# Optimization experiments

Hardware: AMD Instinct MI355X
Metric: run time of the kernel (lower is better)

The kernel has to match this reference:

```python
import jax, jax.numpy as jnp
import numpy as np
from jax import lax

STRIDES = [8, 16, 32, 64, 128]
NUM_CLASSES = 80
PRE_NMS_THRESH = 0.05
PRE_NMS_TOP_N = 1000
NMS_THRESH = 0.6
MAX_DET = 100
IMG_SIZE = 800.0
BBOX_W = (10.0, 10.0, 5.0, 5.0)
SCALE_CLAMP = float(np.log(1000.0 / 16.0))  # Box2BoxTransform clamp


def conv3x3(x, w, b):
    y = lax.conv_general_dilated(x, w, (1, 1), 'SAME',
                                 dimension_numbers=('NCHW', 'OIHW', 'NCHW'))
    return y + b[None, :, None, None]


def conv1x1(x, w, b):
    return jnp.einsum('nchw,kc->nkhw', x, w) + b[None, :, None, None]


def make_anchors(H, W, stride):
    # one square anchor per location, size = 8 * stride (ATSS), offset 0.5
    size = 8.0 * stride
    xs = (jnp.arange(W, dtype=jnp.float32) + 0.5) * stride
    ys = (jnp.arange(H, dtype=jnp.float32) + 0.5) * stride
    cy, cx = jnp.meshgrid(ys, xs, indexing='ij')
    half = size / 2.0
    return jnp.stack([cx - half, cy - half, cx + half, cy + half], -1).reshape(-1, 4)


def decode(deltas, anchors):
    # Box2BoxTransform.apply_deltas with weights (10,10,5,5)
    wx, wy, ww, wh = BBOX_W
    aw = anchors[..., 2] - anchors[..., 0]
    ah = anchors[..., 3] - anchors[..., 1]
    acx = anchors[..., 0] + 0.5 * aw
    acy = anchors[..., 1] + 0.5 * ah
    dx = deltas[..., 0] / wx
    dy = deltas[..., 1] / wy
    dw = jnp.minimum(deltas[..., 2] / ww, SCALE_CLAMP)
    dh = jnp.minimum(deltas[..., 3] / wh, SCALE_CLAMP)
    pcx = dx * aw + acx
    pcy = dy * ah + acy
    pw = jnp.exp(dw) * aw
    ph = jnp.exp(dh) * ah
    boxes = jnp.stack([pcx - 0.5 * pw, pcy - 0.5 * ph,
                       pcx + 0.5 * pw, pcy + 0.5 * ph], -1)
    return jnp.clip(boxes, 0.0, IMG_SIZE)


def iou_one_vs_all(box, boxes):
    x1 = jnp.maximum(box[0], boxes[:, 0])
    y1 = jnp.maximum(box[1], boxes[:, 1])
    x2 = jnp.minimum(box[2], boxes[:, 2])
    y2 = jnp.minimum(box[3], boxes[:, 3])
    inter = jnp.clip(x2 - x1, 0.0) * jnp.clip(y2 - y1, 0.0)
    a1 = (box[2] - box[0]) * (box[3] - box[1])
    a2 = (boxes[:, 2] - boxes[:, 0]) * (boxes[:, 3] - boxes[:, 1])
    return inter / (a1 + a2 - inter + 1e-9)


def nms_single(boxes, scores, classes):
    # class-aware greedy NMS via per-class coordinate offset (ml_nms trick)
    off = classes.astype(boxes.dtype)[:, None] * (2.0 * IMG_SIZE)
    ob = boxes + off

    def step(s, _):
        i = jnp.argmax(s)
        best = s[i]
        iou = iou_one_vs_all(ob[i], ob)
        s = jnp.where(iou > NMS_THRESH, -1.0, s)
        s = s.at[i].set(-1.0)
        return s, (i, best)

    _, (idx, kept) = lax.scan(step, scores, None, length=MAX_DET)
    valid = kept > 0
    out_boxes = jnp.where(valid[:, None], boxes[idx], 0.0)
    out_scores = jnp.where(valid, kept, 0.0)
    out_classes = jnp.where(valid, classes[idx], -1)
    return out_boxes, out_scores, out_classes


def atss_forward(feats, cls_tw, cls_tb, bbox_tw, bbox_tb,
                 wcls, bcls, wbox, bbox_b, wctr, bctr, scales):
    all_boxes, all_scores, all_classes = [], [], []
    for l, x in enumerate(feats):
        c = x
        b = x
        for i in range(cls_tw.shape[0]):  # 4 tower convs
            c = jax.nn.relu(conv3x3(c, cls_tw[i], cls_tb[i]))
            b = jax.nn.relu(conv3x3(b, bbox_tw[i], bbox_tb[i]))
        logits = conv1x1(c, wcls, bcls)               # [N,C,H,W]
        deltas = scales[l] * conv1x1(b, wbox, bbox_b)  # [N,4,H,W]
        ctr = conv1x1(b, wctr, bctr)                   # [N,1,H,W]
        N, C, H, W = logits.shape
        logits = logits.transpose(0, 2, 3, 1).reshape(N, H * W, C)
        deltas = deltas.transpose(0, 2, 3, 1).reshape(N, H * W, 4)
        ctr = ctr.transpose(0, 2, 3, 1).reshape(N, H * W)
        anchors = make_anchors(H, W, STRIDES[l])       # [HW,4]
        # ATSS inference scoring: sigmoid(cls) * sigmoid(centerness)
        s = jax.nn.sigmoid(logits) * jax.nn.sigmoid(ctr)[..., None]
        s = jnp.where(s > PRE_NMS_THRESH, s, 0.0)
        flat = s.reshape(N, -1)                        # [N, HW*C]
        k = min(PRE_NMS_TOP_N, flat.shape[1])
        vals, idx = lax.top_k(flat, k)
        aidx = idx // C
        cidx = idx % C
        d = jnp.take_along_axis(deltas, aidx[:, :, None], axis=1)  # [N,k,4]
        boxes = decode(d, anchors[aidx])
        # final score = sqrt(cls*ctr); safe sqrt to avoid inf grad at 0
        sc = jnp.sqrt(jnp.where(vals > 0, vals, 1.0)) * (vals > 0)
        all_boxes.append(boxes)
        all_scores.append(sc)
        all_classes.append(cidx)
    boxes = jnp.concatenate(all_boxes, 1)
    scores = jnp.concatenate(all_scores, 1)
    classes = jnp.concatenate(all_classes, 1)
    return jax.vmap(nms_single)(boxes, scores, classes)


def setup_inputs() -> dict:
    key = jax.random.key(0)
    ks = jax.random.split(key, 12)
    feats_hw = [(100, 100), (50, 50), (25, 25), (13, 13), (7, 7)]
    N, CIN, CH = 4, 256, 256
    inp = {}
    for i, (h, w) in enumerate(feats_hw):
        inp['p%d' % (i + 3)] = jax.random.normal(ks[i], (N, CIN, h, w), jnp.float32)
    inp['cls_tw'] = jax.random.normal(ks[5], (4, CH, CIN, 3, 3), jnp.float32) * 0.02
    inp['cls_tb'] = jnp.zeros((4, CH), jnp.float32)
    inp['bbox_tw'] = jax.random.normal(ks[6], (4, CH, CIN, 3, 3), jnp.float32) * 0.02
    inp['bbox_tb'] = jnp.zeros((4, CH), jnp.float32)
    inp['wcls'] = jax.random.normal(ks[7], (NUM_CLASSES, CH), jnp.float32) * 0.05
    inp['bcls'] = jnp.zeros((NUM_CLASSES,), jnp.float32)
    inp['wbox'] = jax.random.normal(ks[8], (4, CH), jnp.float32) * 0.05
    inp['bbox_b'] = jnp.zeros((4,), jnp.float32)
    inp['wctr'] = jax.random.normal(ks[9], (1, CH), jnp.float32) * 0.05
    inp['bctr'] = jnp.zeros((1,), jnp.float32)
    inp['scales'] = jnp.ones((5,), jnp.float32)
    return inp


def reference(p3, p4, p5, p6, p7, cls_tw, cls_tb, bbox_tw, bbox_tb,
              wcls, bcls, wbox, bbox_b, wctr, bctr, scales):
    feats = [p3, p4, p5, p6, p7]
    boxes, scores, classes = atss_forward(feats, cls_tw, cls_tb, bbox_tw, bbox_tb,
                                          wcls, bcls, wbox, bbox_b, wctr, bctr, scales)
    return boxes, scores, classes
```

## Files before the change

kernel.cpp:

```cpp
#include <hip/hip_runtime.h>
#include <math.h>

typedef short s8v __attribute__((ext_vector_type(8)));
typedef short s4v __attribute__((ext_vector_type(4)));
typedef float f4v __attribute__((ext_vector_type(4)));
typedef _Float16 h8v __attribute__((ext_vector_type(8)));

__device__ __forceinline__ float sigf(float x) { return 1.f / (1.f + expf(-x)); }
__device__ __forceinline__ float f16f(short v) {
  return (float)__builtin_bit_cast(_Float16, v);
}

#define SCALE_CLAMP 4.135166556742356f
#define IMG_SIZE 800.f
#define PLANE 14482432ull
#define W_SCALE 1024.f
#define A_SCALE 64.f
#define ACC_RESCALE 1.52587890625e-5f

__device__ __forceinline__ void split2(float x, short& h, short& l) {
  _Float16 hf = (_Float16)x;
  _Float16 lf = (_Float16)(x - (float)hf);
  h = __builtin_bit_cast(short, hf);
  l = __builtin_bit_cast(short, lf);
}

struct Geo {
  int tp[6];
  int TXa[5];
  int Ha[5], Wa[5], PWa[5], PHWa[5];
  int phwOff[5];
  int hwOff[5];
  int pb[6];
  int bb[6];
};

__global__ __launch_bounds__(256) void wtrans_k(const float* __restrict__ cls_tw,
                                                const float* __restrict__ bbox_tw,
                                                short* __restrict__ wt)
{
  const int total = 589824;
  for (int u = blockIdx.x * 256 + threadIdx.x; u < total; u += gridDim.x * 256) {
    int layer = u / 73728;
    int r = u - layer * 73728;
    int tap = r / 8192;  r -= tap * 8192;
    int cc  = r / 1024;  r -= cc * 1024;
    int qq  = r / 256;   int ko = r - qq * 256;
    int cibase = cc * 32 + qq * 8;
    const float* src = (layer < 4) ? (cls_tw + (size_t)layer * 589824)
                                   : (bbox_tw + (size_t)(layer - 4) * 589824);
    s8v hv, lv;
#pragma unroll
    for (int e = 0; e < 8; ++e) {
      float x = src[(size_t)ko * 2304 + (size_t)(cibase + e) * 9 + tap] * W_SCALE;
      short h, l; split2(x, h, l);
      hv[e] = h; lv[e] = l;
    }
    size_t dbase = (size_t)layer * 1179648 + (((size_t)tap * 8 + cc) * 4 + qq) * 2048 + (size_t)ko * 8;
    *(s8v*)(wt + dbase) = hv;
    *(s8v*)(wt + dbase + 589824) = lv;
  }
}

__global__ __launch_bounds__(256) void prep_all_k(const float* __restrict__ p3, const float* __restrict__ p4,
                                                  const float* __restrict__ p5, const float* __restrict__ p6,
                                                  const float* __restrict__ p7,
                                                  short* __restrict__ out, Geo g)
{
  __shared__ float tl[64][260];
  int bx = blockIdx.x, t = threadIdx.x, n = blockIdx.y;
  int l = 0; while (l < 4 && bx >= g.pb[l + 1]) ++l;
  const float* in = (l == 0) ? p3 : (l == 1) ? p4 : (l == 2) ? p5 : (l == 3) ? p6 : p7;
  int H = g.Ha[l], W = g.Wa[l], PW = g.PWa[l], PHW = g.PHWa[l], HW = H * W;
  int P0 = (bx - g.pb[l]) * 64;
  const float* inN = in + (size_t)n * HW * 256;
  int sub = t >> 6, pl = t & 63;
  int pos = P0 + pl;
  for (int i = 0; i < 64; ++i) {
    int ci = i * 4 + sub;
    tl[pl][ci] = (pos < HW) ? inN[(size_t)ci * HW + pos] : 0.f;
  }
  __syncthreads();
  int pl2 = t >> 2, cq = (t & 3) * 64;
  int pos2 = P0 + pl2;
  if (pos2 < HW) {
    int y = pos2 / W, x = pos2 - y * W;
    size_t oo = ((size_t)g.phwOff[l] * 4 + (size_t)n * PHW + (size_t)(y + 1) * PW + (x + 1)) * 256 + cq;
#pragma unroll
    for (int grp = 0; grp < 8; ++grp) {
      s8v hv, lv;
#pragma unroll
      for (int e = 0; e < 8; ++e) {
        short h, lo; split2(tl[pl2][cq + grp * 8 + e] * A_SCALE, h, lo);
        hv[e] = h; lv[e] = lo;
      }
      *(s8v*)(out + oo + grp * 8) = hv;
      *(s8v*)(out + PLANE + oo + grp * 8) = lv;
    }
  }
}

#define QS    112
#define QVALID 108
#define PSTR  3584
#define BSTR  7168
__global__ __launch_bounds__(256, 4) void conv_all_k(const short* __restrict__ in0,
                                                     const short* __restrict__ in1,
                                                     const short* __restrict__ wt0,
                                                     const short* __restrict__ wt1,
                                                     const float* __restrict__ bias0,
                                                     const float* __restrict__ bias1,
                                                     short* __restrict__ out0,
                                                     short* __restrict__ out1, Geo g)
{
  __shared__ short act_s[2 * BSTR];

  const int t = threadIdx.x;
  const int lane = t & 63, wave = t >> 6;
  const int wcol = wave & 1, wko = wave >> 1;
  const int tower = blockIdx.z >> 2;
  const int n = blockIdx.z & 3;
  const short* in   = tower ? in1 : in0;
  const short* wtL  = tower ? wt1 : wt0;
  const float* bias = tower ? bias1 : bias0;
  short* out        = tower ? out1 : out0;
  const int ko0 = blockIdx.y * 128;
  int bx = blockIdx.x;
  int l = 0; while (l < 4 && bx >= g.tp[l + 1]) ++l;
  const int H = g.Ha[l], W = g.Wa[l], PW = g.PWa[l], PHW = g.PHWa[l];
  const int lt = bx - g.tp[l];
  const int TX = g.TXa[l];
  const int ty = lt / TX, tx = lt - ty * TX;
  const int R0 = ty * 4, C0 = tx * 16;
  const size_t bi = ((size_t)g.phwOff[l] * 4 + (size_t)n * PHW) * 256;
  const short* inN = in + bi;
  short* outN = out + bi;

  const int r = lane & 15, q = lane >> 4;
  const int cb = wcol * 8;
  const short* wlane = wtL + (size_t)q * 2048 + (size_t)(ko0 + wko * 64 + r) * 8;

  int soff[2];
#pragma unroll
  for (int k = 0; k < 2; ++k) {
    int j = t + k * 256; if (j > 447) j = 447;
    int qq = j / QS, ppos = j - qq * QS;
    int lpos = ppos - 2 * qq; if (lpos < 0) lpos += QS;
    if (lpos >= QVALID) lpos = QVALID - 1;
    int row = lpos / 18, col = lpos - row * 18;
    int prow = R0 + row; if (prow > H + 1) prow = H + 1;
    int pcol = C0 + col; if (pcol > W + 1) pcol = W + 1;
    soff[k] = (prow * PW + pcol) * 256 + qq * 8;
  }

  f4v acc[2][4];
#pragma unroll
  for (int mi = 0; mi < 2; ++mi)
#pragma unroll
    for (int ni = 0; ni < 4; ++ni) { f4v z = {0.f, 0.f, 0.f, 0.f}; acc[mi][ni] = z; }

  auto stage = [&](int cc, int buf) {
#pragma unroll
    for (int k = 0; k < 2; ++k) {
      int j = t + k * 256;
      if (j < 448) {
#pragma unroll
        for (int p = 0; p < 2; ++p) {
          const short* src = inN + (size_t)p * PLANE + (size_t)(soff[k] + cc * 32);
          short* dst = &act_s[(size_t)buf * BSTR + (size_t)p * PSTR + (size_t)j * 8];
#if __has_builtin(__builtin_amdgcn_global_load_lds)
          __builtin_amdgcn_global_load_lds((const __attribute__((address_space(1))) void*)src,
                                           (__attribute__((address_space(3))) void*)dst, 16, 0, 0);
#else
          *(s8v*)dst = *(const s8v*)src;
#endif
        }
      }
    }
  };

  auto loadW = [&](s8v (&w)[2][2], int cc2, int tap2, int half) {
    const short* base = wlane + (size_t)(tap2 * 8 + cc2) * 8192 + half * 256;
#pragma unroll
    for (int p = 0; p < 2; ++p)
#pragma unroll
      for (int k = 0; k < 2; ++k)
        w[p][k] = *(const s8v*)(base + (size_t)p * 589824 + k * 128);
  };

  auto loadA = [&](s8v (&af)[2][2], int dy, int dx, int buf) {
    const int sbase = buf * BSTR;
#pragma unroll
    for (int mi = 0; mi < 2; ++mi) {
      int lp = (2 * mi + (r >> 3) + dy) * 18 + (cb + (r & 7) + dx) + 2 * q;
      if (lp >= QS) lp -= QS;
      int sl = q * QS + lp;
      af[0][mi] = *(const s8v*)&act_s[sbase + sl * 8];
      af[1][mi] = *(const s8v*)&act_s[sbase + PSTR + sl * 8];
    }
  };

  auto runHalf = [&](const s8v (&w)[2][2], const s8v (&af)[2][2], int half) {
    const int PA[3] = {0, 0, 1};
    const int PB[3] = {0, 1, 0};
    __builtin_amdgcn_s_setprio(1);
#pragma unroll
    for (int pp = 0; pp < 3; ++pp)
#pragma unroll
      for (int mi = 0; mi < 2; ++mi)
#pragma unroll
        for (int k = 0; k < 2; ++k)
          acc[mi][half * 2 + k] = __builtin_amdgcn_mfma_f32_16x16x32_f16(
              __builtin_bit_cast(h8v, af[PA[pp]][mi]),
              __builtin_bit_cast(h8v, w[PB[pp]][k]),
              acc[mi][half * 2 + k], 0, 0, 0);
    __builtin_amdgcn_s_setprio(0);
  };

  s8v wH0[2][2], wH1[2][2], afr[2][2];
  stage(0, 0);
  loadW(wH0, 0, 0, 0);
  __syncthreads();

  int cur = 0;
  for (int cc = 0; cc < 8; ++cc) {
    if (cc < 7) stage(cc + 1, cur ^ 1);
#pragma unroll
    for (int tap = 0; tap < 9; ++tap) {
      const int dy = tap / 3, dx = tap - dy * 3;
      loadW(wH1, cc, tap, 1);
      loadA(afr, dy, dx, cur);
      runHalf(wH0, afr, 0);
      int ntap = tap + 1, ncc = cc;
      if (ntap == 9) { ntap = 0; ++ncc; }
      if (ncc < 8) loadW(wH0, ncc, ntap, 0);
      runHalf(wH1, afr, 1);
    }
    __syncthreads();
    cur ^= 1;
  }

#pragma unroll
  for (int mi = 0; mi < 2; ++mi) {
#pragma unroll
    for (int ni = 0; ni < 4; ++ni) {
      int ko = ko0 + wko * 64 + ni * 16 + r;
      float bv = bias[ko];
#pragma unroll
      for (int reg = 0; reg < 4; ++reg) {
        int rm = q * 4 + reg;
        int orow = R0 + 2 * mi + (rm >> 3);
        int ocol = C0 + cb + (rm & 7);
        if (orow < H && ocol < W) {
          float real = acc[mi][ni][reg] * ACC_RESCALE + bv;
          float vv = fmaxf(real, 0.f) * A_SCALE;
          short h, lo; split2(vv, h, lo);
          size_t oo = ((size_t)(orow + 1) * PW + (ocol + 1)) * 256 + ko;
          outN[oo] = h; outN[PLANE + oo] = lo;
        }
      }
    }
  }
}

__global__ __launch_bounds__(256) void cls_head_k(const short* __restrict__ act,
                                                  const float* __restrict__ wcls,
                                                  const float* __restrict__ bcls,
                                                  float* __restrict__ score, Geo g)
{
  __shared__ int   p2s[64];
  __shared__ float as_[64][69];
  __shared__ float ws_[64][84];
  const int t = threadIdx.x;
  const int n = blockIdx.y;
  int bx = blockIdx.x;
  int l = 0; while (l < 4 && bx >= g.pb[l + 1]) ++l;
  const int H = g.Ha[l], W = g.Wa[l], PW = g.PWa[l], PHW = g.PHWa[l], HW = H * W;
  const int P0 = (bx - g.pb[l]) * 64;
  if (t < 64) {
    int p = P0 + t; if (p >= HW) p = HW - 1;
    int y = p / W, x = p - y * W;
    p2s[t] = (y + 1) * PW + x + 1;
  }
  __syncthreads();
  float accv[4][5];
#pragma unroll
  for (int i = 0; i < 4; ++i)
#pragma unroll
    for (int j = 0; j < 5; ++j) accv[i][j] = 0.f;

  const short* actN = act + ((size_t)g.phwOff[l] * 4 + (size_t)n * PHW) * 256;
  const int pg = t >> 4, cg = t & 15;
  const float inv = 1.f / A_SCALE;

  for (int c0 = 0; c0 < 256; c0 += 64) {
    for (int i = t; i < 1024; i += 256) {
      int pos = i >> 4, c4 = i & 15;
      size_t o = (size_t)p2s[pos] * 256 + c0 + c4 * 4;
      s4v hv = *(const s4v*)(actN + o);
      s4v lv = *(const s4v*)(actN + PLANE + o);
      float* dst = &as_[pos][c4 * 4];
#pragma unroll
      for (int e = 0; e < 4; ++e) dst[e] = (f16f(hv[e]) + f16f(lv[e])) * inv;
    }
    for (int i = t; i < 1280; i += 256) {
      int c = i >> 4, c4 = i & 15;
      float4 v = *(const float4*)(wcls + (size_t)c * 256 + c0 + c4 * 4);
      ws_[c4 * 4 + 0][c] = v.x; ws_[c4 * 4 + 1][c] = v.y;
      ws_[c4 * 4 + 2][c] = v.z; ws_[c4 * 4 + 3][c] = v.w;
    }
    __syncthreads();
#pragma unroll 8
    for (int ci = 0; ci < 64; ++ci) {
#pragma unroll
      for (int i = 0; i < 4; ++i) {
        float a = as_[pg * 4 + i][ci];
#pragma unroll
        for (int j = 0; j < 5; ++j)
          accv[i][j] = fmaf(a, ws_[ci][cg * 5 + j], accv[i][j]);
      }
    }
    __syncthreads();
  }
  float* sB = score + ((size_t)g.hwOff[l] * 4 + (size_t)n * HW) * 80;
#pragma unroll
  for (int i = 0; i < 4; ++i) {
    int p = P0 + pg * 4 + i;
    if (p >= HW) continue;
#pragma unroll
    for (int j = 0; j < 5; ++j) {
      int c = cg * 5 + j;
      sB[(size_t)p * 80 + c] = sigf(accv[i][j] + bcls[c]);
    }
  }
}

__global__ __launch_bounds__(256) void box_head_k(const short* __restrict__ act,
                                                  const float* __restrict__ wbox,
                                                  const float* __restrict__ bb,
                                                  const float* __restrict__ wctr,
                                                  const float* __restrict__ bc,
                                                  const float* __restrict__ scales,
                                                  float* __restrict__ score,
                                                  float* __restrict__ deltas, Geo g)
{
  int n = blockIdx.y;
  int bx = blockIdx.x;
  int l = 0; while (l < 4 && bx >= g.bb[l + 1]) ++l;
  const int H = g.Ha[l], W = g.Wa[l], PW = g.PWa[l], PHW = g.PHWa[l], HW = H * W;
  int p = (bx - g.bb[l]) * 256 + threadIdx.x;
  if (p >= HW) return;
  int y = p / W, x = p - y * W;
  const short* a = act + ((size_t)g.phwOff[l] * 4 + (size_t)n * PHW + (size_t)(y + 1) * PW + x + 1) * 256;
  const float inv = 1.f / A_SCALE;
  float d0 = 0, d1 = 0, d2 = 0, d3 = 0, ct = 0;
  for (int gI = 0; gI < 32; ++gI) {
    s8v hv = *(const s8v*)(a + gI * 8);
    s8v lv = *(const s8v*)(a + PLANE + gI * 8);
#pragma unroll
    for (int e = 0; e < 8; ++e) {
      float av = (f16f(hv[e]) + f16f(lv[e])) * inv;
      int c = gI * 8 + e;
      d0 = fmaf(av, wbox[c], d0);
      d1 = fmaf(av, wbox[256 + c], d1);
      d2 = fmaf(av, wbox[512 + c], d2);
      d3 = fmaf(av, wbox[768 + c], d3);
      ct = fmaf(av, wctr[c], ct);
    }
  }
  float sl = scales[l];
  float* dd = deltas + ((size_t)g.hwOff[l] * 4 + (size_t)n * HW + p) * 4;
  dd[0] = sl * (d0 + bb[0]); dd[1] = sl * (d1 + bb[1]);
  dd[2] = sl * (d2 + bb[2]); dd[3] = sl * (d3 + bb[3]);
  float sct = sigf(ct + bc[0]);
  float* sp = score + ((size_t)g.hwOff[l] * 4 + (size_t)n * HW + p) * 80;
#pragma unroll
  for (int i = 0; i < 20; ++i) {
    float4 v = ((float4*)sp)[i];
    v.x *= sct; v.y *= sct; v.z *= sct; v.w *= sct;
    v.x = (v.x > 0.05f) ? v.x : 0.f;
    v.y = (v.y > 0.05f) ? v.y : 0.f;
    v.z = (v.z > 0.05f) ? v.z : 0.f;
    v.w = (v.w > 0.05f) ? v.w : 0.f;
    ((float4*)sp)[i] = v;
  }
}

__global__ __launch_bounds__(256) void hist_k(const float* __restrict__ score,
                                              const unsigned* __restrict__ thr,
                                              unsigned* __restrict__ hist, int phase, Geo g)
{
  const int grp = blockIdx.y;
  const int l = grp >> 2, n = grp & 3;
  const int HW = g.Ha[l] * g.Wa[l];
  const int M = HW * 80;
  const float* s = score + ((size_t)g.hwOff[l] * 4 + (size_t)n * HW) * 80;
  unsigned* h = hist + grp * 2048;
  const unsigned* tr = thr + grp * 8;
  __shared__ unsigned lh[2048];
  for (int i = threadIdx.x; i < 2048; i += 256) lh[i] = 0u;
  __syncthreads();
  unsigned B1 = 0, pref = 0;
  if (phase == 1) B1 = tr[0];
  if (phase == 2) pref = (tr[0] << 11) | tr[1];
  for (int idx = blockIdx.x * 256 + threadIdx.x; idx < M; idx += gridDim.x * 256) {
    float v = s[idx];
    if (v > 0.f) {
      unsigned b = __float_as_uint(v);
      if (phase == 0) atomicAdd(&lh[b >> 20], 1u);
      else if (phase == 1) { if ((b >> 20) == B1) atomicAdd(&lh[(b >> 9) & 0x7FFu], 1u); }
      else { if ((b >> 9) == pref) atomicAdd(&lh[b & 0x1FFu], 1u); }
    }
  }
  __syncthreads();
  for (int i = threadIdx.x; i < 2048; i += 256) { unsigned v = lh[i]; if (v) atomicAdd(&h[i], v); }
}

__global__ __launch_bounds__(256) void scan_k(unsigned* __restrict__ hist,
                                              unsigned* __restrict__ thr, int phase)
{
  const int grp = blockIdx.x, t = threadIdx.x;
  unsigned* h  = hist + grp * 2048;
  unsigned* tr = thr + grp * 8;
  const int nb = (phase == 2) ? 512 : 2048;
  const int PB = nb / 256;
  unsigned target = 1000u;
  bool dead = false;
  if (phase >= 1) {
    target = 1000u - tr[2];
    if (tr[0] == 0xFFFFFFFFu) dead = true;
    if (phase == 2 && tr[1] == 0xFFFFFFFFu) dead = true;
  }
  __shared__ unsigned ps[256];
  __shared__ unsigned s_tot;
  const int hi = nb - t * PB;
  unsigned lsum = 0;
  for (int k = 0; k < PB; ++k) lsum += h[hi - 1 - k];
  ps[t] = lsum;
  __syncthreads();
  if (t == 0) {
    unsigned cum = 0;
    for (int i = 0; i < 256; ++i) { unsigned tmp = ps[i]; ps[i] = cum; cum += tmp; }
    s_tot = cum;
  }
  __syncthreads();
  unsigned exc = ps[t], tot = s_tot;
  if (!dead && tot >= target) {
    if (exc < target && exc + lsum >= target) {
      unsigned cum = exc; int bf = 0; unsigned above = 0;
      for (int k = 0; k < PB; ++k) {
        int bidx = hi - 1 - k;
        unsigned c = h[bidx];
        if (cum < target && cum + c >= target) { bf = bidx; above = cum; }
        cum += c;
      }
      if (phase == 0)      { tr[0] = (unsigned)bf; tr[2] = above; }
      else if (phase == 1) { tr[1] = (unsigned)bf; tr[2] = tr[2] + above; }
      else {
        unsigned T = (tr[0] << 20) | (tr[1] << 9) | (unsigned)bf;
        tr[3] = T; tr[4] = target - above;
      }
    }
  } else if (t == 0) {
    if (phase == 0)      { tr[0] = 0xFFFFFFFFu; tr[2] = 0u; }
    else if (phase == 1) { tr[1] = 0xFFFFFFFFu; }
    else                 { tr[3] = 0u; tr[4] = 0u; }
  }
  if (phase == 2 && t == 0) { tr[5] = 0u; tr[6] = 0u; }
}

__global__ __launch_bounds__(256) void select_k(const float* __restrict__ score,
                                                const float* __restrict__ deltas,
                                                unsigned* __restrict__ thr,
                                                float* __restrict__ cbox, float* __restrict__ csc,
                                                float* __restrict__ ccls, float* __restrict__ cgid,
                                                Geo g)
{
  const int grp = blockIdx.y;
  const int l = grp >> 2, n = grp & 3;
  const int W = g.Wa[l];
  const int HW = g.Ha[l] * W;
  const int M = HW * 80;
  const float stride_ = (float)(8 << l);
  const float* s = score + ((size_t)g.hwOff[l] * 4 + (size_t)n * HW) * 80;
  const float* dBase = deltas + ((size_t)g.hwOff[l] * 4 + (size_t)n * HW) * 4;
  unsigned* tr = thr + grp * 8;
  const unsigned T = tr[3], need = tr[4];
  for (int idx = blockIdx.x * 256 + threadIdx.x; idx < M; idx += gridDim.x * 256) {
    float v = s[idx];
    if (!(v > 0.f)) continue;
    unsigned b = __float_as_uint(v);
    int slot = -1;
    if (b > T) slot = (int)atomicAdd(&tr[5], 1u);
    else if (b == T) {
      unsigned e = atomicAdd(&tr[6], 1u);
      if (e < need) slot = (int)(1000u - need + e);
    }
    if (slot < 0) continue;
    int p = idx / 80, c = idx - p * 80;
    int y = p / W, x = p - y * W;
    const float* d = dBase + (size_t)p * 4;
    float sz  = 8.f * stride_;
    float acx = ((float)x + 0.5f) * stride_;
    float acy = ((float)y + 0.5f) * stride_;
    float dx = d[0] / 10.f, dy = d[1] / 10.f;
    float dw = fminf(d[2] / 5.f, SCALE_CLAMP);
    float dh = fminf(d[3] / 5.f, SCALE_CLAMP);
    float pcx = dx * sz + acx;
    float pcy = dy * sz + acy;
    float pw = expf(dw) * sz;
    float ph = expf(dh) * sz;
    float x1 = pcx - 0.5f * pw, y1_ = pcy - 0.5f * ph;
    float x2 = pcx + 0.5f * pw, y2_ = pcy + 0.5f * ph;
    x1  = fminf(fmaxf(x1, 0.f),  IMG_SIZE);
    y1_ = fminf(fmaxf(y1_, 0.f), IMG_SIZE);
    x2  = fminf(fmaxf(x2, 0.f),  IMG_SIZE);
    y2_ = fminf(fmaxf(y2_, 0.f), IMG_SIZE);
    int cslot = n * 5000 + l * 1000 + slot;
    ((float4*)cbox)[cslot] = make_float4(x1, y1_, x2, y2_);
    csc[cslot]  = sqrtf(v);
    ccls[cslot] = (float)c;
    cgid[cslot] = (float)(((unsigned)l << 20) | (unsigned)idx);
  }
}

__global__ __launch_bounds__(256) void nms_bucket_k(const float* __restrict__ cbox,
                                                    const float* __restrict__ csc,
                                                    const float* __restrict__ ccls,
                                                    const float* __restrict__ cgid,
                                                    float4* __restrict__ bbox2,
                                                    unsigned long long* __restrict__ bkey2,
                                                    int* __restrict__ coff)
{
  __shared__ unsigned cnt[80];
  __shared__ unsigned off_s[81];
  const int n = blockIdx.x, t = threadIdx.x;
  for (int i = t; i < 80; i += 256) cnt[i] = 0u;
  __syncthreads();
  for (int i = t; i < 5000; i += 256) {
    float s = csc[n * 5000 + i];
    if (s > 0.f) atomicAdd(&cnt[(int)ccls[n * 5000 + i]], 1u);
  }
  __syncthreads();
  if (t == 0) {
    unsigned c = 0;
    for (int k = 0; k < 80; ++k) { off_s[k] = c; c += cnt[k]; }
    off_s[80] = c;
  }
  __syncthreads();
  for (int i = t; i < 81; i += 256) coff[n * 81 + i] = (int)off_s[i];
  for (int i = t; i < 80; i += 256) cnt[i] = 0u;
  __syncthreads();
  for (int i = t; i < 5000; i += 256) {
    float s = csc[n * 5000 + i];
    if (s > 0.f) {
      int c = (int)ccls[n * 5000 + i];
      unsigned p = atomicAdd(&cnt[c], 1u);
      int dst = n * 5000 + (int)off_s[c] + (int)p;
      bbox2[dst] = ((const float4*)cbox)[n * 5000 + i];
      unsigned long long sb = (unsigned long long)__float_as_uint(s);
      unsigned gid = (unsigned)cgid[n * 5000 + i];
      bkey2[dst] = (sb << 24) | (unsigned long long)(0xFFFFFFu - gid);
    }
  }
}

__global__ __launch_bounds__(64) void nms_class_k(const float4* __restrict__ bbox2,
                                                  const unsigned long long* __restrict__ bkey2,
                                                  const int* __restrict__ coff,
                                                  float4* __restrict__ kbox,
                                                  unsigned long long* __restrict__ kkey,
                                                  int* __restrict__ kcnt)
{
  __shared__ unsigned long long key_s[5000];
  const int cls = blockIdx.x, n = blockIdx.y, t = threadIdx.x;
  const int lo = coff[n * 81 + cls], hi = coff[n * 81 + cls + 1];
  const int c = hi - lo;
  const int base = n * 5000 + lo;
  for (int i = t; i < c; i += 64) key_s[i] = bkey2[base + i];
  __syncthreads();
  const int outB = (n * 80 + cls) * 100;
  int kept = 0;
  while (kept < 100) {
    unsigned long long best = 0ull; int bi = 0;
    for (int i = t; i < c; i += 64) {
      unsigned long long k = key_s[i];
      if (k > best) { best = k; bi = i; }
    }
#pragma unroll
    for (int o = 32; o; o >>= 1) {
      unsigned long long ok = __shfl_xor(best, o);
      int oi = __shfl_xor(bi, o);
      if (ok > best) { best = ok; bi = oi; }
    }
    if (best == 0ull) break;
    float4 wb = bbox2[base + bi];
    if (t == 0) {
      kbox[outB + kept] = wb;
      kkey[outB + kept] = best;
      key_s[bi] = 0ull;
    }
    ++kept;
    float a1 = (wb.z - wb.x) * (wb.w - wb.y);
    for (int i = t; i < c; i += 64) {
      if (key_s[i] == 0ull) continue;
      float4 b = bbox2[base + i];
      float xx1 = fmaxf(wb.x, b.x), yy1 = fmaxf(wb.y, b.y);
      float xx2 = fminf(wb.z, b.z), yy2 = fminf(wb.w, b.w);
      float inter = fmaxf(xx2 - xx1, 0.f) * fmaxf(yy2 - yy1, 0.f);
      float a2 = (b.z - b.x) * (b.w - b.y);
      float iou = inter / (a1 + a2 - inter + 1e-9f);
      if (iou > 0.6f) key_s[i] = 0ull;
    }
    __syncthreads();
  }
  if (t == 0) kcnt[n * 80 + cls] = kept;
}

__global__ __launch_bounds__(64) void nms_merge_k(const float4* __restrict__ kbox,
                                                  const unsigned long long* __restrict__ kkey,
                                                  const int* __restrict__ kcnt,
                                                  float* __restrict__ outp)
{
  __shared__ int head[80];
  __shared__ int cnts[80];
  const int n = blockIdx.x, t = threadIdx.x;
  for (int i = t; i < 80; i += 64) { head[i] = 0; cnts[i] = kcnt[n * 80 + i]; }
  __syncthreads();
  for (int it = 0; it < 100; ++it) {
    unsigned long long best = 0ull; int bc = 0;
    for (int cls = t; cls < 80; cls += 64) {
      int h = head[cls];
      if (h < cnts[cls]) {
        unsigned long long k = kkey[(n * 80 + cls) * 100 + h];
        if (k > best) { best = k; bc = cls; }
      }
    }
#pragma unroll
    for (int o = 32; o; o >>= 1) {
      unsigned long long ok = __shfl_xor(best, o);
      int oc = __shfl_xor(bc, o);
      if (ok > best) { best = ok; bc = oc; }
    }
    if (t == 0) {
      int basei = n * 100 + it;
      if (best != 0ull) {
        int idx = (n * 80 + bc) * 100 + head[bc];
        float4 b = kbox[idx];
        outp[basei * 4 + 0] = b.x; outp[basei * 4 + 1] = b.y;
        outp[basei * 4 + 2] = b.z; outp[basei * 4 + 3] = b.w;
        outp[1600 + basei] = __uint_as_float((unsigned)(best >> 24));
        outp[2000 + basei] = (float)bc;
        head[bc] = head[bc] + 1;
      } else {
        outp[basei * 4 + 0] = 0.f; outp[basei * 4 + 1] = 0.f;
        outp[basei * 4 + 2] = 0.f; outp[basei * 4 + 3] = 0.f;
        outp[1600 + basei] = 0.f;
        outp[2000 + basei] = -1.f;
      }
    }
    __syncthreads();
  }
}

extern "C" void kernel_launch(void* const* d_in, const int* in_sizes, int n_in,
                              void* d_out, int out_size, void* d_ws, size_t ws_size,
                              hipStream_t stream)
{
  (void)in_sizes; (void)n_in; (void)out_size; (void)ws_size;
  const float* p3 = (const float*)d_in[0];
  const float* p4 = (const float*)d_in[1];
  const float* p5 = (const float*)d_in[2];
  const float* p6 = (const float*)d_in[3];
  const float* p7 = (const float*)d_in[4];
  const float* cls_tw  = (const float*)d_in[5];
  const float* cls_tb  = (const float*)d_in[6];
  const float* bbox_tw = (const float*)d_in[7];
  const float* bbox_tb = (const float*)d_in[8];
  const float* wcls    = (const float*)d_in[9];
  const float* bcls    = (const float*)d_in[10];
  const float* wbox    = (const float*)d_in[11];
  const float* bbox_b  = (const float*)d_in[12];
  const float* wctr    = (const float*)d_in[13];
  const float* bctr    = (const float*)d_in[14];
  const float* scales  = (const float*)d_in[15];
  float* out = (float*)d_out;

  Geo G;
  const int Hs[5] = {100, 50, 25, 13, 7};
  {
    int tpre = 0, ppre = 0, bpre = 0, phw = 0, hw = 0;
    for (int l = 0; l < 5; ++l) {
      int H = Hs[l], W = Hs[l];
      G.Ha[l] = H; G.Wa[l] = W; G.PWa[l] = W + 2; G.PHWa[l] = (H + 2) * (W + 2);
      G.TXa[l] = (W + 15) / 16;
      int TY = (H + 3) / 4;
      G.tp[l] = tpre;  tpre += G.TXa[l] * TY;
      G.pb[l] = ppre;  ppre += (H * W + 63) / 64;
      G.bb[l] = bpre;  bpre += (H * W + 255) / 256;
      G.phwOff[l] = phw; phw += G.PHWa[l];
      G.hwOff[l]  = hw;  hw  += H * W;
    }
    G.tp[5] = tpre; G.pb[5] = ppre; G.bb[5] = bpre;
  }
  const int nTiles = G.tp[5];
  const int nPrep  = G.pb[5];
  const int nBoxB  = G.bb[5];
  const int sumHW = 13343;
  const size_t scoreBytes  = (size_t)sumHW * 4 * 80 * 4;
  const size_t deltasBytes = (size_t)sumHW * 4 * 4 * 4;

  char* ws = (char*)d_ws;
  size_t off = 0;
  auto alloc = [&](size_t bytes) -> void* {
    off = (off + 255) & ~(size_t)255;
    void* p = ws + off; off += bytes; return p;
  };
  const size_t bufBytes = 2ull * PLANE * 2;

  short* wt     = (short*)alloc((size_t)8 * 2 * 589824 * 2);
  float* cbox   = (float*)alloc(4ull * 5000 * 4 * 4);
  float* csc    = (float*)alloc(4ull * 5000 * 4);
  float* ccls   = (float*)alloc(4ull * 5000 * 4);
  float* cgid   = (float*)alloc(4ull * 5000 * 4);
  unsigned* hist = (unsigned*)alloc(20ull * 2048 * 4);
  unsigned* thr  = (unsigned*)alloc(20ull * 8 * 4);
  float4* bbox2 = (float4*)alloc(4ull * 5000 * 16);
  unsigned long long* bkey2 = (unsigned long long*)alloc(4ull * 5000 * 8);
  int* coff     = (int*)alloc(4ull * 81 * 4);
  float4* kbox  = (float4*)alloc(320ull * 100 * 16);
  unsigned long long* kkey = (unsigned long long*)alloc(320ull * 100 * 8);
  int* kcnt     = (int*)alloc(320ull * 4);
  short* A = (short*)alloc(bufBytes);
  short* B = (short*)alloc(bufBytes);
  float* score  = (float*)alloc(scoreBytes);
  float* deltas = (float*)alloc(deltasBytes);

  hipMemsetAsync(csc,  0, 4ull * 5000 * 4, stream);
  hipMemsetAsync(ccls, 0, 4ull * 5000 * 4, stream);
  hipMemsetAsync(cgid, 0, 4ull * 5000 * 4, stream);
  hipMemsetAsync(thr,  0, 20ull * 8 * 4, stream);
  hipMemsetAsync(A, 0, bufBytes, stream);
  hipMemsetAsync(B, 0, bufBytes, stream);

  wtrans_k<<<1024, 256, 0, stream>>>(cls_tw, bbox_tw, wt);

  const size_t LSTRIDE = 2ull * 589824;
  dim3 cg(nTiles, 2, 4);

  prep_all_k<<<dim3(nPrep, 4), 256, 0, stream>>>(p3, p4, p5, p6, p7, A, G);
  conv_all_k<<<cg, 256, 0, stream>>>(A, A, wt + 0 * LSTRIDE, wt + 0 * LSTRIDE,
                                     cls_tb + 0 * 256, cls_tb + 0 * 256, B, B, G);
  conv_all_k<<<cg, 256, 0, stream>>>(B, B, wt + 1 * LSTRIDE, wt + 1 * LSTRIDE,
                                     cls_tb + 1 * 256, cls_tb + 1 * 256, A, A, G);
  conv_all_k<<<cg, 256, 0, stream>>>(A, A, wt + 2 * LSTRIDE, wt + 2 * LSTRIDE,
                                     cls_tb + 2 * 256, cls_tb + 2 * 256, B, B, G);
  conv_all_k<<<cg, 256, 0, stream>>>(B, B, wt + 3 * LSTRIDE, wt + 3 * LSTRIDE,
                                     cls_tb + 3 * 256, cls_tb + 3 * 256, A, A, G);
  cls_head_k<<<dim3(nPrep, 4), 256, 0, stream>>>(A, wcls, bcls, score, G);
  prep_all_k<<<dim3(nPrep, 4), 256, 0, stream>>>(p3, p4, p5, p6, p7, B, G);
  conv_all_k<<<cg, 256, 0, stream>>>(B, B, wt + 4 * LSTRIDE, wt + 4 * LSTRIDE,
                                     bbox_tb + 0 * 256, bbox_tb + 0 * 256, A, A, G);
  conv_all_k<<<cg, 256, 0, stream>>>(A, A, wt + 5 * LSTRIDE, wt + 5 * LSTRIDE,
                                     bbox_tb + 1 * 256, bbox_tb + 1 * 256, B, B, G);
  conv_all_k<<<cg, 256, 0, stream>>>(B, B, wt + 6 * LSTRIDE, wt + 6 * LSTRIDE,
                                     bbox_tb + 2 * 256, bbox_tb + 2 * 256, A, A, G);
  conv_all_k<<<cg, 256, 0, stream>>>(A, A, wt + 7 * LSTRIDE, wt + 7 * LSTRIDE,
                                     bbox_tb + 3 * 256, bbox_tb + 3 * 256, B, B, G);
  box_head_k<<<dim3(nBoxB, 4), 256, 0, stream>>>(B, wbox, bbox_b, wctr, bctr, scales,
                                                 score, deltas, G);

  const int hb = 196;
  for (int phase = 0; phase < 3; ++phase) {
    hipMemsetAsync(hist, 0, 20ull * 2048 * 4, stream);
    hist_k<<<dim3(hb, 20), 256, 0, stream>>>(score, thr, hist, phase, G);
    scan_k<<<20, 256, 0, stream>>>(hist, thr, phase);
  }
  select_k<<<dim3(hb, 20), 256, 0, stream>>>(score, deltas, thr, cbox, csc, ccls, cgid, G);

  nms_bucket_k<<<4, 256, 0, stream>>>(cbox, csc, ccls, cgid, bbox2, bkey2, coff);
  nms_class_k<<<dim3(80, 4), 64, 0, stream>>>(bbox2, bkey2, coff, kbox, kkey, kcnt);
  nms_merge_k<<<4, 64, 0, stream>>>(kbox, kkey, kcnt, out);
}
```

Baseline: 2.269 ms.

## Remap conv grid for XCD locality and rewrite per-class NMS with sorted bitmask scan

The conv launch becomes a 1D grid, and block IDs are remapped so consecutive workgroups on the same XCD (bid&7) handle contiguous tiles and both output-channel halves. This is meant to improve L2 reuse of activations and weights. Per-class NMS now rank-sorts candidates into shared memory once, then walks them in order using ballot scans instead of doing an argmax over all candidates each iteration, with a global-memory fallback for large classes. The merge kernel stages the per-class kept keys in LDS. The O(c^2) rank sort and the larger LDS footprint could cost something for big classes.

```diff
diff --git a/kernel.cpp b/kernel.cpp
--- a/kernel.cpp
+++ b/kernel.cpp
@@ -118,14 +118,18 @@
   const int t = threadIdx.x;
   const int lane = t & 63, wave = t >> 6;
   const int wcol = wave & 1, wko = wave >> 1;
-  const int tower = blockIdx.z >> 2;
-  const int n = blockIdx.z & 3;
-  const short* in   = tower ? in1 : in0;
-  const short* wtL  = tower ? wt1 : wt0;
-  const float* bias = tower ? bias1 : bias0;
-  short* out        = tower ? out1 : out0;
-  const int ko0 = blockIdx.y * 128;
-  int bx = blockIdx.x;
+  const int nT = g.tp[5];
+  int bid = blockIdx.x;
+  int wgid = (bid & 7) * nT + (bid >> 3);
+  const int n = wgid / (2 * nT);
+  int r2 = wgid - n * 2 * nT;
+  int bx = r2 >> 1;
+  const int ko0 = (r2 & 1) * 128;
+  const short* in   = in0;
+  const short* wtL  = wt0;
+  const float* bias = bias0;
+  short* out        = out0;
+  (void)in1; (void)wt1; (void)bias1; (void)out1;
   int l = 0; while (l < 4 && bx >= g.tp[l + 1]) ++l;
   const int H = g.Ha[l], W = g.Wa[l], PW = g.PWa[l], PHW = g.PHWa[l];
   const int lt = bx - g.tp[l];
@@ -565,54 +569,95 @@
   }
 }
 
+#define NCAP 1536
 __global__ __launch_bounds__(64) void nms_class_k(const float4* __restrict__ bbox2,
-                                                  const unsigned long long* __restrict__ bkey2,
+                                                  unsigned long long* __restrict__ bkey2,
                                                   const int* __restrict__ coff,
                                                   float4* __restrict__ kbox,
                                                   unsigned long long* __restrict__ kkey,
                                                   int* __restrict__ kcnt)
 {
-  __shared__ unsigned long long key_s[5000];
+  __shared__ unsigned long long key_s[NCAP];
+  __shared__ unsigned long long sk_s[NCAP];
+  __shared__ float4 sb_s[NCAP];
+  __shared__ unsigned char af_s[NCAP + 64];
   const int cls = blockIdx.x, n = blockIdx.y, t = threadIdx.x;
   const int lo = coff[n * 81 + cls], hi = coff[n * 81 + cls + 1];
   const int c = hi - lo;
   const int base = n * 5000 + lo;
-  for (int i = t; i < c; i += 64) key_s[i] = bkey2[base + i];
-  __syncthreads();
   const int outB = (n * 80 + cls) * 100;
   int kept = 0;
-  while (kept < 100) {
-    unsigned long long best = 0ull; int bi = 0;
+  if (c > 0 && c <= NCAP) {
+    const int nch = (c + 63) >> 6;
+    for (int i = t; i < nch * 64; i += 64) af_s[i] = 0;
+    for (int i = t; i < c; i += 64) key_s[i] = bkey2[base + i];
+    __syncthreads();
     for (int i = t; i < c; i += 64) {
-      unsigned long long k = key_s[i];
-      if (k > best) { best = k; bi = i; }
-    }
-#pragma unroll
-    for (int o = 32; o; o >>= 1) {
-      unsigned long long ok = __shfl_xor(best, o);
-      int oi = __shfl_xor(bi, o);
-      if (ok > best) { best = ok; bi = oi; }
-    }
-    if (best == 0ull) break;
-    float4 wb = bbox2[base + bi];
-    if (t == 0) {
-      kbox[outB + kept] = wb;
-      kkey[outB + kept] = best;
-      key_s[bi] = 0ull;
-    }
-    ++kept;
-    float a1 = (wb.z - wb.x) * (wb.w - wb.y);
-    for (int i = t; i < c; i += 64) {
-      if (key_s[i] == 0ull) continue;
-      float4 b = bbox2[base + i];
-      float xx1 = fmaxf(wb.x, b.x), yy1 = fmaxf(wb.y, b.y);
-      float xx2 = fminf(wb.z, b.z), yy2 = fminf(wb.w, b.w);
-      float inter = fmaxf(xx2 - xx1, 0.f) * fmaxf(yy2 - yy1, 0.f);
-      float a2 = (b.z - b.x) * (b.w - b.y);
-      float iou = inter / (a1 + a2 - inter + 1e-9f);
-      if (iou > 0.6f) key_s[i] = 0ull;
+      unsigned long long ki = key_s[i];
+      int rk = 0;
+      for (int m = 0; m < c; ++m) rk += (key_s[m] > ki) ? 1 : 0;
+      sk_s[rk] = ki;
+      sb_s[rk] = bbox2[base + i];
+      af_s[rk] = 1;
     }
     __syncthreads();
+    int p = -1;
+    while (kept < 100) {
+      int np = -1;
+      int j0 = (p + 1) >> 6;
+      for (int j = j0; j < nch; ++j) {
+        int pos = j * 64 + t;
+        unsigned long long w = __ballot(af_s[pos] != 0);
+        if (j == j0) { int sh = (p + 1) & 63; if (sh) w &= (~0ull) << sh; }
+        if (w) { np = j * 64 + (int)__builtin_ctzll(w); break; }
+      }
+      if (np < 0) break;
+      p = np;
+      float4 wb = sb_s[p];
+      if (t == 0) { kbox[outB + kept] = wb; kkey[outB + kept] = sk_s[p]; }
+      ++kept;
+      float a1 = (wb.z - wb.x) * (wb.w - wb.y);
+      for (int i = p + t; i < c; i += 64) {
+        if (!af_s[i]) continue;
+        float4 b = sb_s[i];
+        float xx1 = fmaxf(wb.x, b.x), yy1 = fmaxf(wb.y, b.y);
+        float xx2 = fminf(wb.z, b.z), yy2 = fminf(wb.w, b.w);
+        float inter = fmaxf(xx2 - xx1, 0.f) * fmaxf(yy2 - yy1, 0.f);
+        float a2 = (b.z - b.x) * (b.w - b.y);
+        if (inter / (a1 + a2 - inter + 1e-9f) > 0.6f) af_s[i] = 0;
+      }
+      __syncthreads();
+    }
+  } else if (c > NCAP) {
+    while (kept < 100) {
+      unsigned long long best = 0ull; int bi = 0;
+      for (int i = t; i < c; i += 64) {
+        unsigned long long k = bkey2[base + i];
+        if (k > best) { best = k; bi = i; }
+      }
+#pragma unroll
+      for (int o = 32; o; o >>= 1) {
+        unsigned long long ok = __shfl_xor(best, o);
+        int oi = __shfl_xor(bi, o);
+        if (ok > best) { best = ok; bi = oi; }
+      }
+      if (best == 0ull) break;
+      float4 wb = bbox2[base + bi];
+      if (t == 0) { kbox[outB + kept] = wb; kkey[outB + kept] = best; }
+      ++kept;
+      float a1 = (wb.z - wb.x) * (wb.w - wb.y);
+      for (int i = t; i < c; i += 64) {
+        unsigned long long k = bkey2[base + i];
+        if (!k) continue;
+        float4 b = bbox2[base + i];
+        float xx1 = fmaxf(wb.x, b.x), yy1 = fmaxf(wb.y, b.y);
+        float xx2 = fminf(wb.z, b.z), yy2 = fminf(wb.w, b.w);
+        float inter = fmaxf(xx2 - xx1, 0.f) * fmaxf(yy2 - yy1, 0.f);
+        float a2 = (b.z - b.x) * (b.w - b.y);
+        if (inter / (a1 + a2 - inter + 1e-9f) > 0.6f) bkey2[base + i] = 0ull;
+      }
+      __syncthreads();
+    }
   }
   if (t == 0) kcnt[n * 80 + cls] = kept;
 }
@@ -622,17 +667,19 @@
                                                   const int* __restrict__ kcnt,
                                                   float* __restrict__ outp)
 {
+  __shared__ unsigned long long lk[8000];
   __shared__ int head[80];
   __shared__ int cnts[80];
   const int n = blockIdx.x, t = threadIdx.x;
   for (int i = t; i < 80; i += 64) { head[i] = 0; cnts[i] = kcnt[n * 80 + i]; }
+  for (int i = t; i < 8000; i += 64) lk[i] = kkey[n * 8000 + i];
   __syncthreads();
   for (int it = 0; it < 100; ++it) {
     unsigned long long best = 0ull; int bc = 0;
     for (int cls = t; cls < 80; cls += 64) {
       int h = head[cls];
       if (h < cnts[cls]) {
-        unsigned long long k = kkey[(n * 80 + cls) * 100 + h];
+        unsigned long long k = lk[cls * 100 + h];
         if (k > best) { best = k; bc = cls; }
       }
     }
@@ -746,7 +793,7 @@
   wtrans_k<<<1024, 256, 0, stream>>>(cls_tw, bbox_tw, wt);
 
   const size_t LSTRIDE = 2ull * 589824;
-  dim3 cg(nTiles, 2, 4);
+  dim3 cg(8 * nTiles);
 
   prep_all_k<<<dim3(nPrep, 4), 256, 0, stream>>>(p3, p4, p5, p6, p7, A, G);
   conv_all_k<<<cg, 256, 0, stream>>>(A, A, wt + 0 * LSTRIDE, wt + 0 * LSTRIDE,
```

After: 2.183 ms. 3.8% less time.
